# Optimization experiments

Hardware: AMD Instinct MI355X
Metric: run time of the kernel (lower is better)

## Reference

```python
import jax, jax.numpy as jnp
import numpy as np

EPS = 1e-5
THRESH = 1.5


def _compute_one(x, g_w, g_b, phi_w, phi_b, W_w, W_b, gamma, beta):
    # x: (c, w, h, z) -- single sample (torch code calls compute_x with batch 1)
    c, w, h, z = x.shape
    nz = z // 2
    # AdaptiveAvgPool3d(1) on x.permute(0,4,2,3,1): mean over (w, h, c) per z-slice -> (z,)
    p = x.mean(axis=(0, 1, 2))
    xp = x * p[None, None, None, :]
    # 1x1x1 conv projections (note: self.theta is defined but unused in the original)
    g_x = jnp.einsum('ic,cwhz->iwhz', g_w, x) + g_b[:, None, None, None]
    phi_x = jnp.einsum('ic,cwhz->iwhz', phi_w, xp) + phi_b[:, None, None, None]
    # MaxPool3d kernel (1,1,2): non-overlapping max pairs along z
    g_x = g_x.reshape(-1, w, h, nz, 2).max(axis=-1)      # (ic, w, h, nz)
    phi_x = phi_x.reshape(-1, w, h, nz, 2).max(axis=-1)  # (ic, w, h, nz)
    # theta_x: (x*p).permute(0,2,3,4,1).view(w*h, z, c)
    theta = xp.transpose(1, 2, 3, 0).reshape(w * h, z, c)
    # phi: permute(0,2,3,1,4).view(w*h, ic, nz)
    phi_m = phi_x.transpose(1, 2, 0, 3).reshape(w * h, -1, nz)
    # g: permute(0,2,3,4,1).view(w*h, nz, ic)
    g_m = g_x.transpose(1, 2, 3, 0).reshape(w * h, nz, -1)
    f = jnp.einsum('bzc,bcn->bzn', theta, phi_m)          # (wh, z, nz)
    a = jax.nn.softmax(f, axis=-1)
    y = jnp.einsum('bzn,bni->bzi', a, g_m)                # (wh, z, ic)
    y = y.reshape(w, h, z, -1).transpose(3, 0, 1, 2)      # (ic, w, h, z)
    wy = jnp.einsum('ci,iwhz->cwhz', W_w, y) + W_b[:, None, None, None]
    # BatchNorm3d in training mode on a single-sample batch: per-channel stats over (w,h,z)
    mu = wy.mean(axis=(1, 2, 3), keepdims=True)
    var = wy.var(axis=(1, 2, 3), keepdims=True)
    wy = (wy - mu) * jax.lax.rsqrt(var + EPS)
    wy = wy * gamma[:, None, None, None] + beta[:, None, None, None]
    return wy + x


def setup_inputs() -> dict:
    key = jax.random.key(0)
    ks = jax.random.split(key, 10)
    b, c, w, h, z = 2, 64, 64, 64, 64
    ic = c  # inter_channels defaults to in_channels
    x = jax.random.normal(ks[0], (b, c, w, h, z), dtype=jnp.float32)
    # spacings in [0, 3): some samples fall above spacing_thresh=1.5 (identity branch)
    spacings = jax.random.uniform(ks[1], (b, 3), dtype=jnp.float32) * 3.0
    g_w = jax.random.normal(ks[2], (ic, c), dtype=jnp.float32) * 0.1
    g_b = jax.random.normal(ks[3], (ic,), dtype=jnp.float32) * 0.1
    phi_w = jax.random.normal(ks[4], (ic, c), dtype=jnp.float32) * 0.1
    phi_b = jax.random.normal(ks[5], (ic,), dtype=jnp.float32) * 0.1
    W_w = jax.random.normal(ks[6], (c, ic), dtype=jnp.float32) * 0.1
    W_b = jax.random.normal(ks[7], (c,), dtype=jnp.float32) * 0.1
    gamma = jax.random.normal(ks[8], (c,), dtype=jnp.float32) * 0.1
    beta = jax.random.normal(ks[9], (c,), dtype=jnp.float32) * 0.1
    return {"x": x, "spacings": spacings, "g_w": g_w, "g_b": g_b,
            "phi_w": phi_w, "phi_b": phi_b, "W_w": W_w, "W_b": W_b,
            "gamma": gamma, "beta": beta}


def reference(x, spacings, g_w, g_b, phi_w, phi_b, W_w, W_b, gamma, beta):
    out = jax.vmap(_compute_one, in_axes=(0,) + (None,) * 8)(
        x, g_w, g_b, phi_w, phi_b, W_w, W_b, gamma, beta)
    use = (spacings[:, -1] <= THRESH)[:, None, None, None, None]
    return jnp.where(use, out, x)
```

## Files before the change

kernel.cpp:

```cpp
#include <hip/hip_runtime.h>
#include <hip/hip_bf16.h>
#include <math.h>

#define THRESH_SP 1.5f
#define WHZc   262144
#define CWHZc  16777216

#define WS_PSUM   0
#define WS_SLOT   128
#define WS_ZERO_N 8320
#define WS_W16_BYTE  65536
#define WS_WY_BYTE   131072
#define WS_W16_NEED  (WS_W16_BYTE + 3u*4096u*2u)
#define WS_WY_NEED   (WS_WY_BYTE + 2u*CWHZc*2u)

typedef __attribute__((ext_vector_type(8))) short bf16x8;
typedef __attribute__((ext_vector_type(4))) float floatx4;
typedef __attribute__((ext_vector_type(4))) float f32x4;
typedef __attribute__((ext_vector_type(2))) unsigned int u32x2;

#define MFMA(a, b, c) __builtin_amdgcn_mfma_f32_16x16x32_bf16((a), (b), (c), 0, 0, 0)

__device__ __forceinline__ unsigned short f2b(float f) {
    __hip_bfloat16 h = __float2bfloat16(f);
    return __builtin_bit_cast(unsigned short, h);
}
__device__ __forceinline__ float b2f(unsigned short h) {
    unsigned int u = ((unsigned int)h) << 16;
    return __builtin_bit_cast(float, u);
}
__device__ __forceinline__ bf16x8 ldfrag(const unsigned short* p, int elem_off) {
    return *(const bf16x8*)(p + elem_off);
}

__global__ __launch_bounds__(256) void k_prep(const float* __restrict__ gw,
                                              const float* __restrict__ pw,
                                              const float* __restrict__ Ww,
                                              float* __restrict__ ws,
                                              unsigned short* __restrict__ w16,
                                              int usew16) {
    const int i = blockIdx.x * 256 + threadIdx.x;
    if (i < WS_ZERO_N) ws[i] = 0.0f;
    if (usew16 && i < 4096) {
        w16[i]        = f2b(gw[i]);
        w16[4096 + i] = f2b(pw[i]);
        w16[8192 + i] = f2b(Ww[i]);
    }
}

__global__ __launch_bounds__(256) void k_pmean(const float* __restrict__ x,
                                               const float* __restrict__ sp,
                                               float* __restrict__ ws) {
    const int b = blockIdx.x >> 9;
    if (sp[b*3 + 2] > THRESH_SP) return;
    const int jb = blockIdx.x & 511;
    __shared__ float s[64];
    const int t = threadIdx.x;
    if (t < 64) s[t] = 0.0f;
    __syncthreads();
    const int idx4 = jb * 256 + t;
    const int z0 = (idx4 & 15) * 4;
    float a0 = 0.f, a1 = 0.f, a2 = 0.f, a3 = 0.f;
    const float* xb = x + (size_t)b * CWHZc;
#pragma unroll 4
    for (int it = 0; it < 32; ++it) {
        const float4 v = *(const float4*)&xb[(size_t)(idx4 + it * 131072) * 4];
        a0 += v.x; a1 += v.y; a2 += v.z; a3 += v.w;
    }
    a0 += __shfl_xor(a0, 16); a0 += __shfl_xor(a0, 32);
    a1 += __shfl_xor(a1, 16); a1 += __shfl_xor(a1, 32);
    a2 += __shfl_xor(a2, 16); a2 += __shfl_xor(a2, 32);
    a3 += __shfl_xor(a3, 16); a3 += __shfl_xor(a3, 32);
    if ((t & 63) < 16) {
        unsafeAtomicAdd(&s[z0 + 0], a0);
        unsafeAtomicAdd(&s[z0 + 1], a1);
        unsafeAtomicAdd(&s[z0 + 2], a2);
        unsafeAtomicAdd(&s[z0 + 3], a3);
    }
    __syncthreads();
    if (t < 64) unsafeAtomicAdd(&ws[WS_PSUM + b * 64 + t], s[t]);
}

#define L_WG     0
#define L_WP     9216
#define L_XA     18432
#define L_GPA    27648
#define L_PHA    32768
#define L_XB     37376
#define L_GPB    46592
#define L_PHB    51712
#define L_ATB    56320
#define L_BIAS   61440
#define L_PS     62208
#define L_TOTAL  62464

__global__ __launch_bounds__(512, 4) void k_main(
    const float* __restrict__ x, const float* __restrict__ sp,
    const float* __restrict__ gw, const float* __restrict__ gb,
    const float* __restrict__ pw, const float* __restrict__ pb,
    const float* __restrict__ Wwp, const float* __restrict__ Wbp,
    float* __restrict__ out, unsigned short* __restrict__ wy16, int use16,
    const unsigned short* __restrict__ w16, int usew16,
    float* __restrict__ ws) {
    const int blk = blockIdx.x;
    const int b = blk >> 11;
    if (sp[b*3 + 2] > THRESH_SP) return;
    const int whpair = (blk & 2047) * 2;

    __shared__ char smem[L_TOTAL];
    unsigned short* wg   = (unsigned short*)(smem + L_WG);
    unsigned short* wp   = (unsigned short*)(smem + L_WP);
    float*          bias = (float*)(smem + L_BIAS);
    float*          p_s  = (float*)(smem + L_PS);
    float*          statsf = (float*)(smem + L_PHA);

    const int t   = threadIdx.x;
    const int wv  = t >> 6;
    const int cid = wv >> 2;
    const int tt  = t & 255;
    const int l   = t & 63;
    const int lr  = l & 15;
    const int lq  = l >> 4;
    const int zt  = (wv & 3) << 4;

    unsigned short* xT   = (unsigned short*)(smem + (cid ? L_XB  : L_XA));
    unsigned short* gpT  = (unsigned short*)(smem + (cid ? L_GPB : L_GPA));
    unsigned short* phpN = (unsigned short*)(smem + (cid ? L_PHB : L_PHA));
    unsigned short* aT   = (unsigned short*)(smem + (cid ? L_ATB : L_WG));

    const int wh    = whpair + cid;
    const int xbase = b * CWHZc + wh * 64;

    {
        const int pr = tt >> 3;
        const int zo = tt & 7;
        const int c0 = pr * 2;
        const float* xc = &x[xbase + c0 * WHZc];
        const float4 A0 = *(const float4*)&xc[zo * 4];
        const float4 A1 = *(const float4*)&xc[zo * 4 + 32];
        const float4 B0 = *(const float4*)&xc[WHZc + zo * 4];
        const float4 B1 = *(const float4*)&xc[WHZc + zo * 4 + 32];
#pragma unroll
        for (int g = 0; g < 2; ++g) {
            const float4 va = g ? A1 : A0;
            const float4 vb = g ? B1 : B0;
            const int zb = (zo + 8 * g) * 4;
            const float av[4] = {va.x, va.y, va.z, va.w};
            const float bw[4] = {vb.x, vb.y, vb.z, vb.w};
#pragma unroll
            for (int j = 0; j < 4; ++j) {
                const int z = zb + j;
                const int chunk = (c0 >> 3) ^ ((z >> 2) & 3);
                const unsigned int pk =
                    (unsigned)f2b(av[j]) | ((unsigned)f2b(bw[j]) << 16);
                *(unsigned int*)&xT[z * 72 + chunk * 8 + (c0 & 7)] = pk;
            }
        }
    }
    if (usew16) {
#pragma unroll
        for (int k = 0; k < 2; ++k) {
            const int f = t + (k << 9);
            const int mat = f >> 9;
            const int i = (f & 511) >> 3, seg = f & 7;
            unsigned short* dst = mat ? wp : wg;
            *(uint4*)&dst[i*72 + seg*8] = *(const uint4*)&w16[mat*4096 + i*64 + seg*8];
        }
    } else {
#pragma unroll
        for (int k = 0; k < 4; ++k) {
            const int f = t + (k << 9);
            const int mat = f >> 10, ff = f & 1023;
            const int i = ff >> 4, c4 = ff & 15;
            const float* src = mat ? pw : gw;
            unsigned short* dst = mat ? wp : wg;
            const float4 v = *(const float4*)&src[i*64 + c4*4];
            uint2 pk;
            pk.x = (unsigned)f2b(v.x) | ((unsigned)f2b(v.y) << 16);
            pk.y = (unsigned)f2b(v.z) | ((unsigned)f2b(v.w) << 16);
            *(uint2*)&dst[i*72 + c4*4] = pk;
        }
    }
    if (t < 192) bias[t] = (t < 64) ? gb[t] : (t < 128) ? pb[t - 64] : Wbp[t - 128];
    if (t < 64)  p_s[t] = ws[WS_PSUM + b*64 + t] * (1.0f / 262144.0f);
    __syncthreads();

    const int zrow  = zt + lr;
    const int abase = zrow * 72 + ((lq ^ ((zrow >> 2) & 3)) << 3);
    const bf16x8 a0 = ldfrag(xT, abase);
    const bf16x8 a1 = ldfrag(xT, abase + 32);
    const float pz0 = p_s[zt + lq*4 + 0], pz1 = p_s[zt + lq*4 + 1];
    const float pz2 = p_s[zt + lq*4 + 2], pz3 = p_s[zt + lq*4 + 3];

    {
        const int n0 = (zt >> 1) + lq*2;
#pragma unroll
        for (int ti = 0; ti < 4; ++ti) {
            const int i = ti*16 + lr;
            const float bv = bias[i];
            floatx4 acc = {bv, bv, bv, bv};
            acc = MFMA(a0, ldfrag(wg, i*72 + lq*8), acc);
            acc = MFMA(a1, ldfrag(wg, i*72 + lq*8 + 32), acc);
            unsigned int pk = (unsigned)f2b(fmaxf(acc[0], acc[1])) |
                              ((unsigned)f2b(fmaxf(acc[2], acc[3])) << 16);
            *(unsigned int*)&gpT[i*40 + n0] = pk;
        }
    }
    __syncthreads();

    {
        const int n0 = (zt >> 1) + lq*2;
#pragma unroll
        for (int ti = 0; ti < 4; ++ti) {
            const int i = ti*16 + lr;
            floatx4 acc = {0.f, 0.f, 0.f, 0.f};
            acc = MFMA(a0, ldfrag(wp, i*72 + lq*8), acc);
            acc = MFMA(a1, ldfrag(wp, i*72 + lq*8 + 32), acc);
            const float bv = bias[64 + i];
            const float v0 = fmaf(acc[0], pz0, bv), v1 = fmaf(acc[1], pz1, bv);
            const float v2 = fmaf(acc[2], pz2, bv), v3 = fmaf(acc[3], pz3, bv);
            phpN[n0*72 + i]       = f2b(fmaxf(v0, v1));
            phpN[(n0 + 1)*72 + i] = f2b(fmaxf(v2, v3));
        }
    }
    __syncthreads();

    {
        floatx4 f0 = {0.f, 0.f, 0.f, 0.f}, f1 = {0.f, 0.f, 0.f, 0.f};
        f0 = MFMA(a0, ldfrag(phpN, lr*72 + lq*8), f0);
        f0 = MFMA(a1, ldfrag(phpN, lr*72 + lq*8 + 32), f0);
        f1 = MFMA(a0, ldfrag(phpN, (16 + lr)*72 + lq*8), f1);
        f1 = MFMA(a1, ldfrag(phpN, (16 + lr)*72 + lq*8 + 32), f1);
        if (usew16) {
            const int i = t >> 3, seg = t & 7;
            *(uint4*)&wp[i*72 + seg*8] = *(const uint4*)&w16[8192 + i*64 + seg*8];
        } else {
#pragma unroll
            for (int k = 0; k < 2; ++k) {
                const int f = t + (k << 9);
                const int i = f >> 4, c4 = f & 15;
                const float4 v = *(const float4*)&Wwp[i*64 + c4*4];
                uint2 pk;
                pk.x = (unsigned)f2b(v.x) | ((unsigned)f2b(v.y) << 16);
                pk.y = (unsigned)f2b(v.z) | ((unsigned)f2b(v.w) << 16);
                *(uint2*)&wp[i*72 + c4*4] = pk;
            }
        }
        const float pz[4] = {pz0, pz1, pz2, pz3};
#pragma unroll
        for (int r = 0; r < 4; ++r) {
            const float fr0 = f0[r] * pz[r], fr1 = f1[r] * pz[r];
            float m = fmaxf(fr0, fr1);
            m = fmaxf(m, __shfl_xor(m, 1)); m = fmaxf(m, __shfl_xor(m, 2));
            m = fmaxf(m, __shfl_xor(m, 4)); m = fmaxf(m, __shfl_xor(m, 8));
            const float e0 = __expf(fr0 - m), e1 = __expf(fr1 - m);
            float s = e0 + e1;
            s += __shfl_xor(s, 1); s += __shfl_xor(s, 2);
            s += __shfl_xor(s, 4); s += __shfl_xor(s, 8);
            const float inv = 1.0f / s;
            const int z = zt + lq*4 + r;
            aT[z*40 + lr]      = f2b(e0 * inv);
            aT[z*40 + lr + 16] = f2b(e1 * inv);
        }
    }
    __syncthreads();

    {
        if (t < 128) statsf[t] = 0.0f;
        const bf16x8 bv = ldfrag(aT, (zt + lr)*40 + lq*8);
        const int zcol = zt + lr;
        const int xzc = (zcol >> 2) & 3;
#pragma unroll
        for (int it = 0; it < 4; ++it) {
            const bf16x8 av = ldfrag(gpT, (it*16 + lr)*40 + lq*8);
            floatx4 acc = {0.f, 0.f, 0.f, 0.f};
            acc = MFMA(av, bv, acc);
            const int i0 = it*16 + lq*4;
            const int chunk = (i0 >> 3) ^ xzc;
            uint2 pk;
            pk.x = (unsigned)f2b(acc[0]) | ((unsigned)f2b(acc[1]) << 16);
            pk.y = (unsigned)f2b(acc[2]) | ((unsigned)f2b(acc[3]) << 16);
            *(uint2*)&xT[zcol*72 + chunk*8 + (i0 & 7)] = pk;
        }
    }
    __syncthreads();

    {
        const bf16x8 y0 = ldfrag(xT, abase);
        const bf16x8 y1 = ldfrag(xT, abase + 32);
#pragma unroll
        for (int ti = 0; ti < 4; ++ti) {
            const int co = ti*16 + lr;
            const float bv = bias[128 + co];
            floatx4 acc = {bv, bv, bv, bv};
            acc = MFMA(y0, ldfrag(wp, co*72 + lq*8), acc);
            acc = MFMA(y1, ldfrag(wp, co*72 + lq*8 + 32), acc);
            if (use16) {
                uint2 pk;
                pk.x = (unsigned)f2b(acc[0]) | ((unsigned)f2b(acc[1]) << 16);
                pk.y = (unsigned)f2b(acc[2]) | ((unsigned)f2b(acc[3]) << 16);
                *(uint2*)&wy16[(size_t)xbase + co * WHZc + zt + lq*4] = pk;
            } else {
                *(float4*)&out[xbase + co * WHZc + zt + lq*4] = *(float4*)&acc;
            }
            float s1 = acc[0] + acc[1] + acc[2] + acc[3];
            float s2 = acc[0]*acc[0] + acc[1]*acc[1] + acc[2]*acc[2] + acc[3]*acc[3];
            s1 += __shfl_xor(s1, 16); s1 += __shfl_xor(s1, 32);
            s2 += __shfl_xor(s2, 16); s2 += __shfl_xor(s2, 32);
            if (lq == 0) {
                atomicAdd(&statsf[co*2],     s1);
                atomicAdd(&statsf[co*2 + 1], s2);
            }
        }
    }
    __syncthreads();
    if (t < 128) {
        const int slot = blk & 31;
        unsafeAtomicAdd(&ws[WS_SLOT + (slot*2 + b)*128 + t], statsf[t]);
    }
}

__global__ __launch_bounds__(256) void k_final(const float* __restrict__ x,
                                               const float* __restrict__ sp,
                                               const float* __restrict__ gamma,
                                               const float* __restrict__ beta,
                                               float* __restrict__ out,
                                               const unsigned short* __restrict__ wy16,
                                               int use16,
                                               const float* __restrict__ ws) {
    const bool use0 = sp[2] <= THRESH_SP;
    const bool use1 = sp[5] <= THRESH_SP;
    __shared__ float scf[128], shf[128];
    if ((use0 || use1) && threadIdx.x < 128) {
        const int t = threadIdx.x;
        const int b = t >> 6, c = t & 63;
        float S1 = 0.f, S2 = 0.f;
        for (int s = 0; s < 32; s++) {
            S1 += ws[WS_SLOT + (s*2 + b)*128 + c*2 + 0];
            S2 += ws[WS_SLOT + (s*2 + b)*128 + c*2 + 1];
        }
        const float N = 262144.0f;
        const float mu = S1 / N;
        const float var = fmaxf(S2 / N - mu * mu, 0.0f);
        const float sc = gamma[c] * rsqrtf(var + 1e-5f);
        scf[t] = sc;
        shf[t] = beta[c] - mu * sc;
    }
    __syncthreads();
    const int nf4 = (2 * CWHZc) / 4;
    for (int i4 = blockIdx.x * blockDim.x + threadIdx.x; i4 < nf4;
         i4 += gridDim.x * blockDim.x) {
        const int idx = i4 * 4;
        const int b = idx >> 24;
        const bool use = b ? use1 : use0;
        const f32x4 xv = __builtin_nontemporal_load((const f32x4*)&x[idx]);
        f32x4 ov;
        if (use) {
            const int c = (idx >> 18) & 63;
            const float scv = scf[b * 64 + c];
            const float shv = shf[b * 64 + c];
            float w0, w1, w2, w3;
            if (use16) {
                const u32x2 q = __builtin_nontemporal_load((const u32x2*)&wy16[idx]);
                w0 = b2f((unsigned short)(q.x & 0xffffu));
                w1 = b2f((unsigned short)(q.x >> 16));
                w2 = b2f((unsigned short)(q.y & 0xffffu));
                w3 = b2f((unsigned short)(q.y >> 16));
            } else {
                const float4 wy = *(const float4*)&out[idx];
                w0 = wy.x; w1 = wy.y; w2 = wy.z; w3 = wy.w;
            }
            ov.x = w0 * scv + shv + xv.x;
            ov.y = w1 * scv + shv + xv.y;
            ov.z = w2 * scv + shv + xv.z;
            ov.w = w3 * scv + shv + xv.w;
        } else {
            ov = xv;
        }
        __builtin_nontemporal_store(ov, (f32x4*)&out[idx]);
    }
}

extern "C" void kernel_launch(void* const* d_in, const int* in_sizes, int n_in,
                              void* d_out, int out_size, void* d_ws, size_t ws_size,
                              hipStream_t stream) {
    const float* x     = (const float*)d_in[0];
    const float* spv   = (const float*)d_in[1];
    const float* gw    = (const float*)d_in[2];
    const float* gb    = (const float*)d_in[3];
    const float* pw    = (const float*)d_in[4];
    const float* pb    = (const float*)d_in[5];
    const float* Ww    = (const float*)d_in[6];
    const float* Wb    = (const float*)d_in[7];
    const float* gamma = (const float*)d_in[8];
    const float* beta  = (const float*)d_in[9];
    float* out = (float*)d_out;
    float* ws  = (float*)d_ws;
    const int usew16 = (ws_size >= (size_t)WS_W16_NEED) ? 1 : 0;
    const int use16  = (ws_size >= (size_t)WS_WY_NEED) ? 1 : 0;
    unsigned short* w16  = (unsigned short*)((char*)d_ws + WS_W16_BYTE);
    unsigned short* wy16 = (unsigned short*)((char*)d_ws + WS_WY_BYTE);

    k_prep<<<48, 256, 0, stream>>>(gw, pw, Ww, ws, w16, usew16);
    k_pmean<<<1024, 256, 0, stream>>>(x, spv, ws);
    k_main<<<4096, 512, 0, stream>>>(x, spv, gw, gb, pw, pb, Ww, Wb,
                                     out, wy16, use16, w16, usew16, ws);
    k_final<<<2048, 256, 0, stream>>>(x, spv, gamma, beta, out, wy16, use16, ws);
}
```

Baseline: 129.3 us.

## Shrink main kernel to one wh column per block and split BN stats kernel

The main kernel now handles one (w,h) column per 256-thread block instead of two per 512-thread block. It drops the staged weight and bias tiles in shared memory and reads bf16 weight fragments and biases straight from global/L2, which removes several block barriers and lowers LDS use so more blocks fit per CU. The mean-pool kernel switches to contiguous per-block chunks. BN scale/shift computation moves into a separate single-block kernel, and the final kernel becomes a per-block channel-uniform loop with a copy fast path for skipped samples. The costs are more global loads of weights per wave and an extra kernel launch.

```diff
diff --git a/kernel.cpp b/kernel.cpp
--- a/kernel.cpp
+++ b/kernel.cpp
@@ -8,6 +8,8 @@
 
 #define WS_PSUM   0
 #define WS_SLOT   128
+#define WS_SC     8320
+#define WS_SH     8448
 #define WS_ZERO_N 8320
 #define WS_W16_BYTE  65536
 #define WS_WY_BYTE   131072
@@ -31,6 +33,14 @@
 }
 __device__ __forceinline__ bf16x8 ldfrag(const unsigned short* p, int elem_off) {
     return *(const bf16x8*)(p + elem_off);
+}
+__device__ __forceinline__ bf16x8 wfrag(const unsigned short* wm, const float* wf,
+                                        int usew16, int row, int k0) {
+    if (usew16) return *(const bf16x8*)(wm + row * 64 + k0);
+    bf16x8 r;
+#pragma unroll
+    for (int j = 0; j < 8; ++j) r[j] = (short)f2b(wf[row * 64 + k0 + j]);
+    return r;
 }
 
 __global__ __launch_bounds__(256) void k_prep(const float* __restrict__ gw,
@@ -51,20 +61,19 @@
 __global__ __launch_bounds__(256) void k_pmean(const float* __restrict__ x,
                                                const float* __restrict__ sp,
                                                float* __restrict__ ws) {
-    const int b = blockIdx.x >> 9;
+    const int blk = blockIdx.x;
+    const int b = blk >> 10;
     if (sp[b*3 + 2] > THRESH_SP) return;
-    const int jb = blockIdx.x & 511;
     __shared__ float s[64];
     const int t = threadIdx.x;
     if (t < 64) s[t] = 0.0f;
     __syncthreads();
-    const int idx4 = jb * 256 + t;
-    const int z0 = (idx4 & 15) * 4;
+    const int base4 = blk * 4096;
+    const int z0 = (t & 15) * 4;
     float a0 = 0.f, a1 = 0.f, a2 = 0.f, a3 = 0.f;
-    const float* xb = x + (size_t)b * CWHZc;
 #pragma unroll 4
-    for (int it = 0; it < 32; ++it) {
-        const float4 v = *(const float4*)&xb[(size_t)(idx4 + it * 131072) * 4];
+    for (int k = 0; k < 16; ++k) {
+        const float4 v = *(const float4*)&x[(size_t)(base4 + k*256 + t) * 4];
         a0 += v.x; a1 += v.y; a2 += v.z; a3 += v.w;
     }
     a0 += __shfl_xor(a0, 16); a0 += __shfl_xor(a0, 32);
@@ -81,20 +90,7 @@
     if (t < 64) unsafeAtomicAdd(&ws[WS_PSUM + b * 64 + t], s[t]);
 }
 
-#define L_WG     0
-#define L_WP     9216
-#define L_XA     18432
-#define L_GPA    27648
-#define L_PHA    32768
-#define L_XB     37376
-#define L_GPB    46592
-#define L_PHB    51712
-#define L_ATB    56320
-#define L_BIAS   61440
-#define L_PS     62208
-#define L_TOTAL  62464
-
-__global__ __launch_bounds__(512, 4) void k_main(
+__global__ __launch_bounds__(256, 6) void k_main(
     const float* __restrict__ x, const float* __restrict__ sp,
     const float* __restrict__ gw, const float* __restrict__ gb,
     const float* __restrict__ pw, const float* __restrict__ pb,
@@ -103,37 +99,26 @@
     const unsigned short* __restrict__ w16, int usew16,
     float* __restrict__ ws) {
     const int blk = blockIdx.x;
-    const int b = blk >> 11;
+    const int b = blk >> 12;
     if (sp[b*3 + 2] > THRESH_SP) return;
-    const int whpair = (blk & 2047) * 2;
-
-    __shared__ char smem[L_TOTAL];
-    unsigned short* wg   = (unsigned short*)(smem + L_WG);
-    unsigned short* wp   = (unsigned short*)(smem + L_WP);
-    float*          bias = (float*)(smem + L_BIAS);
-    float*          p_s  = (float*)(smem + L_PS);
-    float*          statsf = (float*)(smem + L_PHA);
-
-    const int t   = threadIdx.x;
-    const int wv  = t >> 6;
-    const int cid = wv >> 2;
-    const int tt  = t & 255;
-    const int l   = t & 63;
-    const int lr  = l & 15;
-    const int lq  = l >> 4;
-    const int zt  = (wv & 3) << 4;
-
-    unsigned short* xT   = (unsigned short*)(smem + (cid ? L_XB  : L_XA));
-    unsigned short* gpT  = (unsigned short*)(smem + (cid ? L_GPB : L_GPA));
-    unsigned short* phpN = (unsigned short*)(smem + (cid ? L_PHB : L_PHA));
-    unsigned short* aT   = (unsigned short*)(smem + (cid ? L_ATB : L_WG));
-
-    const int wh    = whpair + cid;
+    const int wh = blk & 4095;
     const int xbase = b * CWHZc + wh * 64;
 
-    {
-        const int pr = tt >> 3;
-        const int zo = tt & 7;
+    __shared__ unsigned short xT[64 * 72];
+    __shared__ unsigned short gpT[64 * 40];
+    __shared__ unsigned short phpN[32 * 72];
+    __shared__ unsigned short aT[64 * 40];
+    __shared__ float statsf[128];
+
+    const int t  = threadIdx.x;
+    const int l  = t & 63;
+    const int lr = l & 15;
+    const int lq = l >> 4;
+    const int zt = (t >> 6) << 4;
+
+    {
+        const int pr = t >> 3;
+        const int zo = t & 7;
         const int c0 = pr * 2;
         const float* xc = &x[xbase + c0 * WHZc];
         const float4 A0 = *(const float4*)&xc[zo * 4];
@@ -156,69 +141,38 @@
                 *(unsigned int*)&xT[z * 72 + chunk * 8 + (c0 & 7)] = pk;
             }
         }
-    }
-    if (usew16) {
-#pragma unroll
-        for (int k = 0; k < 2; ++k) {
-            const int f = t + (k << 9);
-            const int mat = f >> 9;
-            const int i = (f & 511) >> 3, seg = f & 7;
-            unsigned short* dst = mat ? wp : wg;
-            *(uint4*)&dst[i*72 + seg*8] = *(const uint4*)&w16[mat*4096 + i*64 + seg*8];
-        }
-    } else {
-#pragma unroll
-        for (int k = 0; k < 4; ++k) {
-            const int f = t + (k << 9);
-            const int mat = f >> 10, ff = f & 1023;
-            const int i = ff >> 4, c4 = ff & 15;
-            const float* src = mat ? pw : gw;
-            unsigned short* dst = mat ? wp : wg;
-            const float4 v = *(const float4*)&src[i*64 + c4*4];
-            uint2 pk;
-            pk.x = (unsigned)f2b(v.x) | ((unsigned)f2b(v.y) << 16);
-            pk.y = (unsigned)f2b(v.z) | ((unsigned)f2b(v.w) << 16);
-            *(uint2*)&dst[i*72 + c4*4] = pk;
-        }
-    }
-    if (t < 192) bias[t] = (t < 64) ? gb[t] : (t < 128) ? pb[t - 64] : Wbp[t - 128];
-    if (t < 64)  p_s[t] = ws[WS_PSUM + b*64 + t] * (1.0f / 262144.0f);
+        if (t < 128) statsf[t] = 0.0f;
+    }
     __syncthreads();
 
     const int zrow  = zt + lr;
     const int abase = zrow * 72 + ((lq ^ ((zrow >> 2) & 3)) << 3);
     const bf16x8 a0 = ldfrag(xT, abase);
     const bf16x8 a1 = ldfrag(xT, abase + 32);
-    const float pz0 = p_s[zt + lq*4 + 0], pz1 = p_s[zt + lq*4 + 1];
-    const float pz2 = p_s[zt + lq*4 + 2], pz3 = p_s[zt + lq*4 + 3];
+    const float pinv = 1.0f / 262144.0f;
+    const float pz0 = ws[WS_PSUM + b*64 + zt + lq*4 + 0] * pinv;
+    const float pz1 = ws[WS_PSUM + b*64 + zt + lq*4 + 1] * pinv;
+    const float pz2 = ws[WS_PSUM + b*64 + zt + lq*4 + 2] * pinv;
+    const float pz3 = ws[WS_PSUM + b*64 + zt + lq*4 + 3] * pinv;
 
     {
         const int n0 = (zt >> 1) + lq*2;
 #pragma unroll
         for (int ti = 0; ti < 4; ++ti) {
             const int i = ti*16 + lr;
-            const float bv = bias[i];
-            floatx4 acc = {bv, bv, bv, bv};
-            acc = MFMA(a0, ldfrag(wg, i*72 + lq*8), acc);
-            acc = MFMA(a1, ldfrag(wg, i*72 + lq*8 + 32), acc);
-            unsigned int pk = (unsigned)f2b(fmaxf(acc[0], acc[1])) |
-                              ((unsigned)f2b(fmaxf(acc[2], acc[3])) << 16);
+            const float gbv = gb[i];
+            floatx4 accg = {gbv, gbv, gbv, gbv};
+            accg = MFMA(a0, wfrag(w16, gw, usew16, i, lq*8), accg);
+            accg = MFMA(a1, wfrag(w16, gw, usew16, i, lq*8 + 32), accg);
+            unsigned int pk = (unsigned)f2b(fmaxf(accg[0], accg[1])) |
+                              ((unsigned)f2b(fmaxf(accg[2], accg[3])) << 16);
             *(unsigned int*)&gpT[i*40 + n0] = pk;
-        }
-    }
-    __syncthreads();
-
-    {
-        const int n0 = (zt >> 1) + lq*2;
-#pragma unroll
-        for (int ti = 0; ti < 4; ++ti) {
-            const int i = ti*16 + lr;
-            floatx4 acc = {0.f, 0.f, 0.f, 0.f};
-            acc = MFMA(a0, ldfrag(wp, i*72 + lq*8), acc);
-            acc = MFMA(a1, ldfrag(wp, i*72 + lq*8 + 32), acc);
-            const float bv = bias[64 + i];
-            const float v0 = fmaf(acc[0], pz0, bv), v1 = fmaf(acc[1], pz1, bv);
-            const float v2 = fmaf(acc[2], pz2, bv), v3 = fmaf(acc[3], pz3, bv);
+            floatx4 accp = {0.f, 0.f, 0.f, 0.f};
+            accp = MFMA(a0, wfrag(w16 + 4096, pw, usew16, i, lq*8), accp);
+            accp = MFMA(a1, wfrag(w16 + 4096, pw, usew16, i, lq*8 + 32), accp);
+            const float pbv = pb[i];
+            const float v0 = fmaf(accp[0], pz0, pbv), v1 = fmaf(accp[1], pz1, pbv);
+            const float v2 = fmaf(accp[2], pz2, pbv), v3 = fmaf(accp[3], pz3, pbv);
             phpN[n0*72 + i]       = f2b(fmaxf(v0, v1));
             phpN[(n0 + 1)*72 + i] = f2b(fmaxf(v2, v3));
         }
@@ -231,21 +185,6 @@
         f0 = MFMA(a1, ldfrag(phpN, lr*72 + lq*8 + 32), f0);
         f1 = MFMA(a0, ldfrag(phpN, (16 + lr)*72 + lq*8), f1);
         f1 = MFMA(a1, ldfrag(phpN, (16 + lr)*72 + lq*8 + 32), f1);
-        if (usew16) {
-            const int i = t >> 3, seg = t & 7;
-            *(uint4*)&wp[i*72 + seg*8] = *(const uint4*)&w16[8192 + i*64 + seg*8];
-        } else {
-#pragma unroll
-            for (int k = 0; k < 2; ++k) {
-                const int f = t + (k << 9);
-                const int i = f >> 4, c4 = f & 15;
-                const float4 v = *(const float4*)&Wwp[i*64 + c4*4];
-                uint2 pk;
-                pk.x = (unsigned)f2b(v.x) | ((unsigned)f2b(v.y) << 16);
-                pk.y = (unsigned)f2b(v.z) | ((unsigned)f2b(v.w) << 16);
-                *(uint2*)&wp[i*72 + c4*4] = pk;
-            }
-        }
         const float pz[4] = {pz0, pz1, pz2, pz3};
 #pragma unroll
         for (int r = 0; r < 4; ++r) {
@@ -263,10 +202,8 @@
             aT[z*40 + lr + 16] = f2b(e1 * inv);
         }
     }
-    __syncthreads();
-
-    {
-        if (t < 128) statsf[t] = 0.0f;
+
+    {
         const bf16x8 bv = ldfrag(aT, (zt + lr)*40 + lq*8);
         const int zcol = zt + lr;
         const int xzc = (zcol >> 2) & 3;
@@ -283,7 +220,6 @@
             *(uint2*)&xT[zcol*72 + chunk*8 + (i0 & 7)] = pk;
         }
     }
-    __syncthreads();
 
     {
         const bf16x8 y0 = ldfrag(xT, abase);
@@ -291,10 +227,10 @@
 #pragma unroll
         for (int ti = 0; ti < 4; ++ti) {
             const int co = ti*16 + lr;
-            const float bv = bias[128 + co];
+            const float bv = Wbp[co];
             floatx4 acc = {bv, bv, bv, bv};
-            acc = MFMA(y0, ldfrag(wp, co*72 + lq*8), acc);
-            acc = MFMA(y1, ldfrag(wp, co*72 + lq*8 + 32), acc);
+            acc = MFMA(y0, wfrag(w16 + 8192, Wwp, usew16, co, lq*8), acc);
+            acc = MFMA(y1, wfrag(w16 + 8192, Wwp, usew16, co, lq*8 + 32), acc);
             if (use16) {
                 uint2 pk;
                 pk.x = (unsigned)f2b(acc[0]) | ((unsigned)f2b(acc[1]) << 16);
@@ -320,63 +256,69 @@
     }
 }
 
+__global__ __launch_bounds__(128) void k_stats(const float* __restrict__ gamma,
+                                               const float* __restrict__ beta,
+                                               float* __restrict__ ws) {
+    const int t = threadIdx.x;
+    if (t >= 128) return;
+    const int b = t >> 6, c = t & 63;
+    float S1 = 0.f, S2 = 0.f;
+    for (int s = 0; s < 32; s++) {
+        S1 += ws[WS_SLOT + (s*2 + b)*128 + c*2 + 0];
+        S2 += ws[WS_SLOT + (s*2 + b)*128 + c*2 + 1];
+    }
+    const float N = 262144.0f;
+    const float mu = S1 / N;
+    const float var = fmaxf(S2 / N - mu * mu, 0.0f);
+    const float sc = gamma[c] * rsqrtf(var + 1e-5f);
+    ws[WS_SC + t] = sc;
+    ws[WS_SH + t] = beta[c] - mu * sc;
+}
+
 __global__ __launch_bounds__(256) void k_final(const float* __restrict__ x,
                                                const float* __restrict__ sp,
-                                               const float* __restrict__ gamma,
-                                               const float* __restrict__ beta,
                                                float* __restrict__ out,
                                                const unsigned short* __restrict__ wy16,
                                                int use16,
                                                const float* __restrict__ ws) {
-    const bool use0 = sp[2] <= THRESH_SP;
-    const bool use1 = sp[5] <= THRESH_SP;
-    __shared__ float scf[128], shf[128];
-    if ((use0 || use1) && threadIdx.x < 128) {
-        const int t = threadIdx.x;
-        const int b = t >> 6, c = t & 63;
-        float S1 = 0.f, S2 = 0.f;
-        for (int s = 0; s < 32; s++) {
-            S1 += ws[WS_SLOT + (s*2 + b)*128 + c*2 + 0];
-            S2 += ws[WS_SLOT + (s*2 + b)*128 + c*2 + 1];
-        }
-        const float N = 262144.0f;
-        const float mu = S1 / N;
-        const float var = fmaxf(S2 / N - mu * mu, 0.0f);
-        const float sc = gamma[c] * rsqrtf(var + 1e-5f);
-        scf[t] = sc;
-        shf[t] = beta[c] - mu * sc;
-    }
-    __syncthreads();
-    const int nf4 = (2 * CWHZc) / 4;
-    for (int i4 = blockIdx.x * blockDim.x + threadIdx.x; i4 < nf4;
-         i4 += gridDim.x * blockDim.x) {
-        const int idx = i4 * 4;
-        const int b = idx >> 24;
-        const bool use = b ? use1 : use0;
+    const int blk = blockIdx.x;
+    const int b = blk >> 10;
+    const bool use = sp[b*3 + 2] <= THRESH_SP;
+    const int base4 = blk * 4096;
+    const int t = threadIdx.x;
+    if (!use) {
+#pragma unroll 4
+        for (int k = 0; k < 16; ++k) {
+            const int i4 = base4 + k*256 + t;
+            const f32x4 xv = __builtin_nontemporal_load((const f32x4*)&x[(size_t)i4*4]);
+            __builtin_nontemporal_store(xv, (f32x4*)&out[(size_t)i4*4]);
+        }
+        return;
+    }
+    const int c = (blk & 1023) >> 4;
+    const float scv = ws[WS_SC + b*64 + c];
+    const float shv = ws[WS_SH + b*64 + c];
+#pragma unroll 4
+    for (int k = 0; k < 16; ++k) {
+        const int i4 = base4 + k*256 + t;
+        const size_t idx = (size_t)i4 * 4;
         const f32x4 xv = __builtin_nontemporal_load((const f32x4*)&x[idx]);
         f32x4 ov;
-        if (use) {
-            const int c = (idx >> 18) & 63;
-            const float scv = scf[b * 64 + c];
-            const float shv = shf[b * 64 + c];
-            float w0, w1, w2, w3;
-            if (use16) {
-                const u32x2 q = __builtin_nontemporal_load((const u32x2*)&wy16[idx]);
-                w0 = b2f((unsigned short)(q.x & 0xffffu));
-                w1 = b2f((unsigned short)(q.x >> 16));
-                w2 = b2f((unsigned short)(q.y & 0xffffu));
-                w3 = b2f((unsigned short)(q.y >> 16));
-            } else {
-                const float4 wy = *(const float4*)&out[idx];
-                w0 = wy.x; w1 = wy.y; w2 = wy.z; w3 = wy.w;
-            }
-            ov.x = w0 * scv + shv + xv.x;
-            ov.y = w1 * scv + shv + xv.y;
-            ov.z = w2 * scv + shv + xv.z;
-            ov.w = w3 * scv + shv + xv.w;
+        float w0, w1, w2, w3;
+        if (use16) {
+            const u32x2 q = __builtin_nontemporal_load((const u32x2*)&wy16[idx]);
+            w0 = b2f((unsigned short)(q.x & 0xffffu));
+            w1 = b2f((unsigned short)(q.x >> 16));
+            w2 = b2f((unsigned short)(q.y & 0xffffu));
+            w3 = b2f((unsigned short)(q.y >> 16));
         } else {
-            ov = xv;
-        }
+            const float4 wy = *(const float4*)&out[idx];
+            w0 = wy.x; w1 = wy.y; w2 = wy.z; w3 = wy.w;
+        }
+        ov.x = w0 * scv + shv + xv.x;
+        ov.y = w1 * scv + shv + xv.y;
+        ov.z = w2 * scv + shv + xv.z;
+        ov.w = w3 * scv + shv + xv.w;
         __builtin_nontemporal_store(ov, (f32x4*)&out[idx]);
     }
 }
@@ -402,8 +344,9 @@
     unsigned short* wy16 = (unsigned short*)((char*)d_ws + WS_WY_BYTE);
 
     k_prep<<<48, 256, 0, stream>>>(gw, pw, Ww, ws, w16, usew16);
-    k_pmean<<<1024, 256, 0, stream>>>(x, spv, ws);
-    k_main<<<4096, 512, 0, stream>>>(x, spv, gw, gb, pw, pb, Ww, Wb,
+    k_pmean<<<2048, 256, 0, stream>>>(x, spv, ws);
+    k_main<<<8192, 256, 0, stream>>>(x, spv, gw, gb, pw, pb, Ww, Wb,
                                      out, wy16, use16, w16, usew16, ws);
-    k_final<<<2048, 256, 0, stream>>>(x, spv, gamma, beta, out, wy16, use16, ws);
-}
+    k_stats<<<1, 128, 0, stream>>>(gamma, beta, ws);
+    k_final<<<2048, 256, 0, stream>>>(x, spv, out, wy16, use16, ws);
+}
```

Result: slower. 153.4 us (+18.6%).
